# Optimization experiments

Hardware: AMD Instinct MI355X
Metric: run time of the kernel (lower is better)

Reference implementation:

```python
import jax, jax.numpy as jnp
import numpy as np

MAX_ITER = 16
TOL = 1e-3


def setup_inputs() -> dict:
    key = jax.random.key(0)
    k0, k1, k2, k3 = jax.random.split(key, 4)
    B, A, Bd, Y = 16384, 1024, 2, 128
    AT = jax.random.uniform(k0, (B, A), dtype=jnp.float32)
    K = jax.random.uniform(k1, (A, Bd), dtype=jnp.float32)
    BT = jnp.ones((Bd,), dtype=jnp.float32)  # fixed to [1, 1] in the module
    u = jax.random.uniform(k2, (A * Bd, Y), dtype=jnp.float32)
    b = jax.random.uniform(k3, (Y,), dtype=jnp.float32)
    return {"AT": AT, "K": K, "BT": BT, "u": u, "b": b}


def reference(AT, K, BT, u, b):
    batch = AT.shape[0]
    Kp = K ** 2  # 'reparam' constraint

    # Fixed-point matrix-balancing loop (torch.no_grad block) -> constants.
    Ksg = jax.lax.stop_gradient(Kp)
    ATsg = jax.lax.stop_gradient(AT)
    A_dim, B_dim = Kp.shape
    af0 = jnp.zeros((batch, A_dim), jnp.float32)
    bf0 = jnp.zeros((batch, B_dim), jnp.float32)

    def cond(carry):
        _, _, err, i = carry
        return (i < MAX_ITER) & (err >= TOL)

    def body(carry):
        af, bf, _, i = carry
        af_n = ATsg / (bf @ Ksg.T + 1.0)   # (batch, A_dim)
        bf_n = BT / (af_n @ Ksg + 1.0)     # (batch, B_dim)
        err = jnp.max(jnp.abs(af_n - af)) + jnp.max(jnp.abs(bf_n - bf))
        return af_n, bf_n, err, i + 1

    _, bf, _, _ = jax.lax.while_loop(
        cond, body, (af0, bf0, jnp.array(jnp.inf, jnp.float32), 0)
    )
    bf = jax.lax.stop_gradient(bf)

    # Final differentiable iteration.
    af = AT / (bf @ Kp.T + 1.0)            # (batch, A_dim)
    bf = BT / (af @ Kp + 1.0)              # (batch, B_dim)

    # C = K * (AF @ BF^T): rank-1 outer product per batch element.
    C = (Kp[None, :, :] * af[:, :, None] * bf[:, None, :]).reshape(batch, -1)
    return C @ u + b
```

## Files before the change

kernel.cpp:

```cpp
#include <hip/hip_runtime.h>

__device__ __forceinline__ unsigned short f2b(float f) {
    unsigned int u = __builtin_bit_cast(unsigned int, f);
    u += 0x7fffu + ((u >> 16) & 1u);
    return (unsigned short)(u >> 16);
}
__device__ __forceinline__ float fastrcp(float x) {
    return __builtin_amdgcn_rcpf(x);
}
__device__ __forceinline__ unsigned int cvt_pk_bf16(float lo, float hi) {
    unsigned int r;
    asm("v_cvt_pk_bf16_f32 %0, %1, %2" : "=v"(r) : "v"(lo), "v"(hi));
    return r;
}
template<int CTRL>
__device__ __forceinline__ float dpp_add(float x) {
    int s = __builtin_amdgcn_update_dpp(0, __builtin_bit_cast(int, x), CTRL, 0xf, 0xf, true);
    return x + __builtin_bit_cast(float, s);
}
__device__ __forceinline__ float wave_sum_bcast(float x) {
    x = dpp_add<0x111>(x);
    x = dpp_add<0x112>(x);
    x = dpp_add<0x114>(x);
    x = dpp_add<0x118>(x);
    x = dpp_add<0x142>(x);
    x = dpp_add<0x143>(x);
    return __builtin_bit_cast(float,
        __builtin_amdgcn_readlane(__builtin_bit_cast(int, x), 63));
}

typedef short bf16x8_t __attribute__((ext_vector_type(8)));
typedef float f32x4_t  __attribute__((ext_vector_type(4)));

#define LDS_PTR(p) ((__attribute__((address_space(3))) void*)(p))
#define GLB_PTR(p) ((const __attribute__((address_space(1))) void*)(p))

#define NB   16384
#define AD   1024
#define YD   128

__global__ __launch_bounds__(256) void vt_kernel(
    const float* __restrict__ Kq,
    const float* __restrict__ U,
    unsigned short* __restrict__ Vtf)
{
    int o  = blockIdx.x * 256 + threadIdx.x;
    int T  = o >> 14;
    int CQ = (o >> 7) & 127;
    int rr = (o >> 3) & 15;
    int e  = o & 7;
    int n  = T * 16 + rr;
    int a  = CQ * 8 + e;
    int j  = n >> 7;
    int y  = n & 127;
    float k  = Kq[2 * a + j];
    float uv = U[(size_t)(2 * a + j) * YD + y];
    Vtf[o] = f2b(k * k * uv);
}

__global__ __launch_bounds__(512, 4) void row_kernel(
    const float* __restrict__ AT,
    const float* __restrict__ Kq,
    const float* __restrict__ BTv,
    unsigned short* __restrict__ afb,
    float* __restrict__ bff)
{
    const int t    = threadIdx.x;
    const int lane = t & 63;
    const int w    = t >> 6;
    const int R0   = blockIdx.x * 16 + w * 2;

    float kp0[16], kp1[16];
#pragma unroll
    for (int c = 0; c < 4; ++c) {
        int base = c * 256 + lane * 4;
        float4 k0v = *(const float4*)(Kq + 2 * base);
        float4 k1v = *(const float4*)(Kq + 2 * base + 4);
        kp0[c * 4 + 0] = k0v.x * k0v.x; kp1[c * 4 + 0] = k0v.y * k0v.y;
        kp0[c * 4 + 1] = k0v.z * k0v.z; kp1[c * 4 + 1] = k0v.w * k0v.w;
        kp0[c * 4 + 2] = k1v.x * k1v.x; kp1[c * 4 + 2] = k1v.y * k1v.y;
        kp0[c * 4 + 3] = k1v.z * k1v.z; kp1[c * 4 + 3] = k1v.w * k1v.w;
    }
    const float bt0 = BTv[0], bt1 = BTv[1];

    const float* atb = AT + (size_t)R0 * AD;

    float ta[2][16];
#pragma unroll
    for (int r = 0; r < 2; ++r) {
#pragma unroll
        for (int c = 0; c < 4; ++c) {
            float4 av = *(const float4*)(atb + (size_t)r * AD + c * 256 + lane * 4);
            ta[r][c * 4 + 0] = av.x; ta[r][c * 4 + 1] = av.y;
            ta[r][c * 4 + 2] = av.z; ta[r][c * 4 + 3] = av.w;
        }
    }

#pragma unroll
    for (int r = 0; r < 2; ++r) {
        float M[9];
#pragma unroll
        for (int i2 = 0; i2 < 9; ++i2) M[i2] = 0.f;
#pragma unroll
        for (int e = 0; e < 16; ++e) {
            float tv = ta[r][e], p = kp0[e], q2 = kp1[e];
            float u0 = tv * p, u1 = tv * q2;
            M[0] += u0; M[1] += u1;
            float u00 = u0 * p, u01 = u0 * q2, u11 = u1 * q2;
            M[2] += u00; M[3] += u01; M[4] += u11;
            M[5] += u00 * p; M[6] += u00 * q2; M[7] += u01 * q2; M[8] += u11 * q2;
        }
#pragma unroll
        for (int i2 = 0; i2 < 9; ++i2) M[i2] = wave_sum_bcast(M[i2]);

        float bf0 = 0.f, bf1 = 0.f;
#pragma unroll
        for (int it = 0; it < 8; ++it) {
            float q00 = bf0 * bf0, q01 = bf0 * bf1, q11 = bf1 * bf1;
            float s0 = M[0] - (bf0 * M[2] + bf1 * M[3]) + (q00 * M[5] + 2.f * q01 * M[6] + q11 * M[7]);
            float s1 = M[1] - (bf0 * M[3] + bf1 * M[4]) + (q00 * M[6] + 2.f * q01 * M[7] + q11 * M[8]);
            bf0 = bt0 * fastrcp(1.f + s0);
            bf1 = bt1 * fastrcp(1.f + s1);
        }
        const int R = R0 + r;
        if (lane == 0) { bff[(size_t)R * 2] = bf0; bff[(size_t)R * 2 + 1] = bf1; }

        unsigned short* base = afb + (size_t)(R >> 5) * 32768 + (size_t)(R & 31) * 1024;
        const int s7 = R & 7;
#pragma unroll
        for (int c = 0; c < 4; ++c) {
            float v[4];
#pragma unroll
            for (int e = 0; e < 4; ++e) {
                int idx = c * 4 + e;
                v[e] = ta[r][idx] * fastrcp(1.f + bf0 * kp0[idx] + bf1 * kp1[idx]);
            }
            uint2 pk;
            pk.x = cvt_pk_bf16(v[0], v[1]);
            pk.y = cvt_pk_bf16(v[2], v[3]);
            int cg = c * 4 + (lane >> 4);
            int cl = (lane >> 1) & 7;
            int off = (cg * 8 + (cl ^ s7)) * 8 + (lane & 1) * 4;
            *(uint2*)(base + off) = pk;
        }
    }
}

__global__ __launch_bounds__(512, 4) void gemm_kernel(
    const unsigned short* __restrict__ afb,
    const unsigned short* __restrict__ Vtf,
    const float* __restrict__ bff,
    const float* __restrict__ bias,
    float* __restrict__ out)
{
    __shared__ __align__(16) unsigned short lA[32 * 1024];

    const int t    = threadIdx.x;
    const int lane = t & 63;
    const int w    = t >> 6;
    const int mtile = blockIdx.x;

    const unsigned short* img = afb + (size_t)mtile * 32768;
#pragma unroll
    for (int i = 0; i < 8; ++i) {
        int s = i * 512 + t;
        __builtin_amdgcn_global_load_lds(GLB_PTR(img + s * 8), LDS_PTR(&lA[s * 8]), 16, 0, 0);
    }
    __syncthreads();

    const int rr = lane & 15;
    const int hb = lane >> 4;
    const int rx = rr & 7;

    const unsigned short* pB = Vtf + (size_t)w * 16384 + hb * 128 + rr * 8;

    f32x4_t acc[2][2];
#pragma unroll
    for (int i = 0; i < 2; ++i)
#pragma unroll
        for (int j = 0; j < 2; ++j) acc[i][j] = (f32x4_t){0.f, 0.f, 0.f, 0.f};

    bf16x8_t fbA[2], fbB[2];

    auto loadB = [&](bf16x8_t* fb, int k0, int kk) {
        int ke = k0 * 16 + kk * 512;
        fb[0] = *(const bf16x8_t*)(pB + ke);
        fb[1] = *(const bf16x8_t*)(pB + ke + 131072);
    };
    auto compute = [&](const bf16x8_t* fb, int k0, int kk) {
        const int cq = kk * 4 + hb;
        bf16x8_t fa[2];
#pragma unroll
        for (int i = 0; i < 2; ++i)
            fa[i] = *(const bf16x8_t*)(
                &lA[(((i * 16 + rr) * 128) + (k0 >> 6) * 8 + (cq ^ rx)) * 8]);
#pragma unroll
        for (int i = 0; i < 2; ++i)
#pragma unroll
            for (int j = 0; j < 2; ++j)
                acc[i][j] = __builtin_amdgcn_mfma_f32_16x16x32_bf16(fa[i], fb[j], acc[i][j], 0, 0, 0);
    };

    loadB(fbA, 0, 0);
    loadB(fbB, 0, 1);
#pragma unroll 1
    for (int k0 = 0; k0 < AD; k0 += 64) {
        __builtin_amdgcn_s_setprio(1);
        compute(fbA, k0, 0);
        __builtin_amdgcn_s_setprio(0);
        if (k0 + 64 < AD) loadB(fbA, k0 + 64, 0);
        __builtin_amdgcn_s_setprio(1);
        compute(fbB, k0, 1);
        __builtin_amdgcn_s_setprio(0);
        if (k0 + 64 < AD) loadB(fbB, k0 + 64, 1);
    }

    const int y  = w * 16 + rr;
    const float bv = bias[y];
#pragma unroll
    for (int i = 0; i < 2; ++i) {
        int mbase = mtile * 32 + i * 16 + hb * 4;
        float2 bfv[4];
#pragma unroll
        for (int r = 0; r < 4; ++r)
            bfv[r] = *(const float2*)(bff + (size_t)(mbase + r) * 2);
#pragma unroll
        for (int r = 0; r < 4; ++r) {
            float val = bfv[r].x * acc[i][0][r] + bfv[r].y * acc[i][1][r] + bv;
            out[(size_t)(mbase + r) * YD + y] = val;
        }
    }
}

extern "C" void kernel_launch(void* const* d_in, const int* in_sizes, int n_in,
                              void* d_out, int out_size, void* d_ws, size_t ws_size,
                              hipStream_t stream) {
    const float* AT  = (const float*)d_in[0];
    const float* Kq  = (const float*)d_in[1];
    const float* BTv = (const float*)d_in[2];
    const float* U   = (const float*)d_in[3];
    const float* bia = (const float*)d_in[4];
    float* out = (float*)d_out;

    char* ws = (char*)d_ws;
    unsigned short* Vtf = (unsigned short*)ws;
    unsigned short* afb = (unsigned short*)(ws + 524288);
    float*          bff = (float*)(ws + 524288 + 33554432);

    vt_kernel <<<dim3(1024), dim3(256), 0, stream>>>(Kq, U, Vtf);
    row_kernel <<<dim3(NB / 16), dim3(512), 0, stream>>>(AT, Kq, BTv, afb, bff);
    gemm_kernel<<<dim3(NB / 32), dim3(512), 0, stream>>>(afb, Vtf, bff, bia, out);
}
```

Measured before the change: 126.0 us.

## Enlarge GEMM M-tile to 64 rows with split-K LDS staging overlap

Each GEMM block now covers 64 batch rows instead of 32. Its 8 waves split as 2 row-halves by 4 column groups, and each wave computes 4 B fragments so every B load feeds twice as many MFMAs. The A tile is staged into LDS in two K-halves, and the second half's load overlaps compute on the first. The cost is doubled LDS use (128KB), fewer blocks per CU, more accumulator registers, and half as many blocks in the grid.

```diff
diff --git a/kernel.cpp b/kernel.cpp
--- a/kernel.cpp
+++ b/kernel.cpp
@@ -146,68 +146,93 @@
     }
 }
 
-__global__ __launch_bounds__(512, 4) void gemm_kernel(
+__global__ __launch_bounds__(512, 2) void gemm_kernel(
     const unsigned short* __restrict__ afb,
     const unsigned short* __restrict__ Vtf,
     const float* __restrict__ bff,
     const float* __restrict__ bias,
     float* __restrict__ out)
 {
-    __shared__ __align__(16) unsigned short lA[32 * 1024];
+    __shared__ __align__(16) unsigned short lA[64 * 1024];
 
     const int t    = threadIdx.x;
     const int lane = t & 63;
     const int w    = t >> 6;
     const int mtile = blockIdx.x;
 
-    const unsigned short* img = afb + (size_t)mtile * 32768;
-#pragma unroll
-    for (int i = 0; i < 8; ++i) {
-        int s = i * 512 + t;
-        __builtin_amdgcn_global_load_lds(GLB_PTR(img + s * 8), LDS_PTR(&lA[s * 8]), 16, 0, 0);
-    }
-    __syncthreads();
+    const unsigned short* img = afb + (size_t)mtile * 65536;
+
+    auto stage = [&](int hh) {
+#pragma unroll
+        for (int i = 0; i < 8; ++i) {
+            int s = i * 512 + t;
+            int off = (s >> 6) * 1024 + hh * 512 + (s & 63) * 8;
+            __builtin_amdgcn_global_load_lds(GLB_PTR(img + off), LDS_PTR(&lA[off]), 16, 0, 0);
+        }
+    };
 
     const int rr = lane & 15;
     const int hb = lane >> 4;
     const int rx = rr & 7;
-
-    const unsigned short* pB = Vtf + (size_t)w * 16384 + hb * 128 + rr * 8;
-
-    f32x4_t acc[2][2];
+    const int q  = w & 3;
+    const int h  = w >> 2;
+
+    const unsigned short* pB = Vtf + (size_t)q * 16384 + hb * 128 + rr * 8;
+
+    stage(0);
+
+    f32x4_t acc[2][4];
 #pragma unroll
     for (int i = 0; i < 2; ++i)
 #pragma unroll
-        for (int j = 0; j < 2; ++j) acc[i][j] = (f32x4_t){0.f, 0.f, 0.f, 0.f};
-
-    bf16x8_t fbA[2], fbB[2];
+        for (int j = 0; j < 4; ++j) acc[i][j] = (f32x4_t){0.f, 0.f, 0.f, 0.f};
+
+    bf16x8_t fbA[4], fbB[4];
 
     auto loadB = [&](bf16x8_t* fb, int k0, int kk) {
         int ke = k0 * 16 + kk * 512;
         fb[0] = *(const bf16x8_t*)(pB + ke);
-        fb[1] = *(const bf16x8_t*)(pB + ke + 131072);
+        fb[1] = *(const bf16x8_t*)(pB + ke + 65536);
+        fb[2] = *(const bf16x8_t*)(pB + ke + 131072);
+        fb[3] = *(const bf16x8_t*)(pB + ke + 196608);
     };
     auto compute = [&](const bf16x8_t* fb, int k0, int kk) {
         const int cq = kk * 4 + hb;
         bf16x8_t fa[2];
 #pragma unroll
+        for (int i = 0; i < 2; ++i) {
+            int r = h * 32 + i * 16 + rr;
+            fa[i] = *(const bf16x8_t*)(&lA[((r * 128) + (k0 >> 6) * 8 + (cq ^ rx)) * 8]);
+        }
+#pragma unroll
         for (int i = 0; i < 2; ++i)
-            fa[i] = *(const bf16x8_t*)(
-                &lA[(((i * 16 + rr) * 128) + (k0 >> 6) * 8 + (cq ^ rx)) * 8]);
-#pragma unroll
-        for (int i = 0; i < 2; ++i)
-#pragma unroll
-            for (int j = 0; j < 2; ++j)
+#pragma unroll
+            for (int j = 0; j < 4; ++j)
                 acc[i][j] = __builtin_amdgcn_mfma_f32_16x16x32_bf16(fa[i], fb[j], acc[i][j], 0, 0, 0);
     };
 
     loadB(fbA, 0, 0);
     loadB(fbB, 0, 1);
+    __syncthreads();
+    stage(1);
+
 #pragma unroll 1
-    for (int k0 = 0; k0 < AD; k0 += 64) {
+    for (int k0 = 0; k0 < 512; k0 += 64) {
         __builtin_amdgcn_s_setprio(1);
         compute(fbA, k0, 0);
         __builtin_amdgcn_s_setprio(0);
+        loadB(fbA, k0 + 64, 0);
+        __builtin_amdgcn_s_setprio(1);
+        compute(fbB, k0, 1);
+        __builtin_amdgcn_s_setprio(0);
+        loadB(fbB, k0 + 64, 1);
+    }
+    __syncthreads();
+#pragma unroll 1
+    for (int k0 = 512; k0 < AD; k0 += 64) {
+        __builtin_amdgcn_s_setprio(1);
+        compute(fbA, k0, 0);
+        __builtin_amdgcn_s_setprio(0);
         if (k0 + 64 < AD) loadB(fbA, k0 + 64, 0);
         __builtin_amdgcn_s_setprio(1);
         compute(fbB, k0, 1);
@@ -215,19 +240,22 @@
         if (k0 + 64 < AD) loadB(fbB, k0 + 64, 1);
     }
 
-    const int y  = w * 16 + rr;
-    const float bv = bias[y];
 #pragma unroll
     for (int i = 0; i < 2; ++i) {
-        int mbase = mtile * 32 + i * 16 + hb * 4;
+        int mbase = mtile * 64 + h * 32 + i * 16 + hb * 4;
         float2 bfv[4];
 #pragma unroll
         for (int r = 0; r < 4; ++r)
             bfv[r] = *(const float2*)(bff + (size_t)(mbase + r) * 2);
 #pragma unroll
-        for (int r = 0; r < 4; ++r) {
-            float val = bfv[r].x * acc[i][0][r] + bfv[r].y * acc[i][1][r] + bv;
-            out[(size_t)(mbase + r) * YD + y] = val;
+        for (int jj = 0; jj < 2; ++jj) {
+            int y = q * 16 + jj * 64 + rr;
+            float bv = bias[y];
+#pragma unroll
+            for (int r = 0; r < 4; ++r) {
+                float val = bfv[r].x * acc[i][jj][r] + bfv[r].y * acc[i][jj + 2][r] + bv;
+                out[(size_t)(mbase + r) * YD + y] = val;
+            }
         }
     }
 }
@@ -249,5 +277,5 @@
 
     vt_kernel <<<dim3(1024), dim3(256), 0, stream>>>(Kq, U, Vtf);
     row_kernel <<<dim3(NB / 16), dim3(512), 0, stream>>>(AT, Kq, BTv, afb, bff);
-    gemm_kernel<<<dim3(NB / 32), dim3(512), 0, stream>>>(afb, Vtf, bff, bia, out);
-}
+    gemm_kernel<<<dim3(NB / 64), dim3(512), 0, stream>>>(afb, Vtf, bff, bia, out);
+}
```

Result: no change. 127.0 us (+0.9%).
